# Optimization experiments

Hardware: AMD Instinct MI355X
Metric: run time of the kernel (lower is better)

## Reference

```python
import jax, jax.numpy as jnp
import numpy as np

D_IN, D, N_HEADS, K, VOCAB = 768, 512, 8, 6, 1000
HEAD_DIM = D // N_HEADS


def setup_inputs() -> dict:
    key = jax.random.key(0)
    ks = jax.random.split(key, 16)
    B, T, L = 32, 4096, 512
    s = 0.02
    return {
        "video_features": jax.random.normal(ks[0], (B, T, D_IN), jnp.float32),
        "input_ids": jax.random.randint(ks[1], (B, L), 0, VOCAB),
        "attention_mask": jnp.ones((B, L), jnp.float32),
        # video_encoder (Linear 768->512), stored [in, out]
        "W_enc": jax.random.normal(ks[2], (D_IN, D), jnp.float32) * s,
        "b_enc": jnp.zeros((D,), jnp.float32),
        # frame_selector (Linear 512->1)
        "W_sel": jax.random.normal(ks[3], (D, 1), jnp.float32) * s,
        "b_sel": jnp.zeros((1,), jnp.float32),
        # text_encoder embedding
        "emb": jax.random.normal(ks[4], (VOCAB, D), jnp.float32) * s,
        # MultiheadAttention in/out projections
        "W_q": jax.random.normal(ks[5], (D, D), jnp.float32) * s,
        "W_k": jax.random.normal(ks[6], (D, D), jnp.float32) * s,
        "W_v": jax.random.normal(ks[7], (D, D), jnp.float32) * s,
        "b_q": jnp.zeros((D,), jnp.float32),
        "b_k": jnp.zeros((D,), jnp.float32),
        "b_v": jnp.zeros((D,), jnp.float32),
        "W_o": jax.random.normal(ks[8], (D, D), jnp.float32) * s,
        "b_o": jnp.zeros((D,), jnp.float32),
        # classifier (Linear 512->1000)
        "W_cls": jax.random.normal(ks[9], (D, VOCAB), jnp.float32) * s,
        "b_cls": jnp.zeros((VOCAB,), jnp.float32),
    }


def reference(video_features, input_ids, attention_mask, W_enc, b_enc, W_sel,
              b_sel, emb, W_q, W_k, W_v, b_q, b_k, b_v, W_o, b_o, W_cls, b_cls):
    # encode frames: [B, T, 512]
    ve = jax.nn.relu(jnp.einsum('bti,io->bto', video_features, W_enc) + b_enc)
    # frame scores [B, T] -> top-6 gather
    scores = jnp.einsum('btd,do->bto', ve, W_sel)[..., 0] + b_sel[0]
    _, top_idx = jax.lax.top_k(scores, K)                      # [B, K]
    reps = jnp.take_along_axis(ve, top_idx[:, :, None], axis=1)  # [B, K, 512]
    # text embedding (query), reps as key/value
    txt = emb[input_ids]                                       # [B, L, 512]
    B, L, _ = txt.shape
    q = (txt @ W_q + b_q).reshape(B, L, N_HEADS, HEAD_DIM)
    k = (reps @ W_k + b_k).reshape(B, K, N_HEADS, HEAD_DIM)
    v = (reps @ W_v + b_v).reshape(B, K, N_HEADS, HEAD_DIM)
    scale = 1.0 / np.sqrt(HEAD_DIM).astype(np.float32)
    attn = jax.nn.softmax(jnp.einsum('blhd,bkhd->bhlk', q, k) * scale, axis=-1)
    ctx = jnp.einsum('bhlk,bkhd->blhd', attn, v).reshape(B, L, D)
    fused = ctx @ W_o + b_o
    logits = fused @ W_cls + b_cls                             # [B, L, 1000]
    return logits, reps
```

## Files before the change

### kernel.cpp

```cpp
#include <hip/hip_runtime.h>
#include <math.h>


#define DEV __device__ __forceinline__

typedef _Float16 half8 __attribute__((ext_vector_type(8)));
typedef float f32x4v __attribute__((ext_vector_type(4)));

DEV unsigned short f2h_bits(float f) {
  union { _Float16 h; unsigned short u; } cv;
  cv.h = (_Float16)f;
  return cv.u;
}

DEV void gload16(const void* g, void* lds) {
  auto* gp = reinterpret_cast<const __attribute__((address_space(1))) unsigned int*>(
      reinterpret_cast<unsigned long long>(g));
  auto* lp = reinterpret_cast<__attribute__((address_space(3))) unsigned int*>(
      reinterpret_cast<unsigned long long>(lds));
  __builtin_amdgcn_global_load_lds(gp, lp, 16, 0, 0);
}

__global__ __launch_bounds__(256) void wenct_k(const float* __restrict__ W_enc,
                                               unsigned short* __restrict__ WencT) {
  __shared__ unsigned short t[64][65];
  const int k0 = blockIdx.x * 64, n0 = blockIdx.y * 64, tid = threadIdx.x;
  for (int e = tid; e < 4096; e += 256) {
    int kk = e >> 6, nn = e & 63;
    t[kk][nn] = f2h_bits(W_enc[(size_t)(k0 + kk) * 512 + n0 + nn]);
  }
  __syncthreads();
  for (int e = tid; e < 4096; e += 256) {
    int nn = e >> 6, kk = e & 63;
    WencT[(size_t)(n0 + nn) * 768 + k0 + kk] = t[kk][nn];
  }
}

__global__ __launch_bounds__(512, 2) void score_gemm(
    const float* __restrict__ vf, const unsigned short* __restrict__ WencT,
    const float* __restrict__ b_enc, const float* __restrict__ W_sel,
    const float* __restrict__ b_sel, float* __restrict__ scores) {
  __shared__ unsigned short As[128 * 64];
  __shared__ unsigned short Bs[512 * 64];
  __shared__ float red[8 * 128];

  const int tid = threadIdx.x;
  const int w = tid >> 6, lane = tid & 63;
  const int quad = lane >> 4, l15 = lane & 15;
  const int rowBase = blockIdx.x * 128;
  const int swz = l15 & 7;
  char* const AsB = (char*)As;
  char* const BsB = (char*)Bs;

  f32x4v acc[8][4];
#pragma unroll
  for (int i = 0; i < 8; ++i)
#pragma unroll
    for (int j = 0; j < 4; ++j) acc[i][j] = (f32x4v){0.f, 0.f, 0.f, 0.f};

  const int ar0 = tid >> 3, as0 = tid & 7;

  for (int kk = 0; kk < 12; ++kk) {
    const int k0 = kk * 64;
    __syncthreads();
#pragma unroll
    for (int it = 0; it < 8; ++it) {
      int q = tid + it * 512;
      int n = q >> 3, seg = q & 7;
      gload16(WencT + (size_t)n * 768 + k0 + ((seg ^ (n & 7)) << 3),
              BsB + (it * 512 + w * 64) * 16);
    }
#pragma unroll
    for (int h = 0; h < 2; ++h) {
      int row = ar0 + h * 64;
      const float* src = vf + (size_t)(rowBase + row) * 768 + k0 + as0 * 8;
      float4 fa = *(const float4*)src;
      float4 fb = *(const float4*)(src + 4);
      uint4 pk;
      pk.x = f2h_bits(fa.x) | ((unsigned int)f2h_bits(fa.y) << 16);
      pk.y = f2h_bits(fa.z) | ((unsigned int)f2h_bits(fa.w) << 16);
      pk.z = f2h_bits(fb.x) | ((unsigned int)f2h_bits(fb.y) << 16);
      pk.w = f2h_bits(fb.z) | ((unsigned int)f2h_bits(fb.w) << 16);
      *(uint4*)(AsB + row * 128 + ((as0 ^ (row & 7)) << 4)) = pk;
    }
    __syncthreads();
#pragma unroll
    for (int c = 0; c < 2; ++c) {
      half8 af[8], bfr[4];
      const int so = (((c << 2) | quad) ^ swz) << 4;
#pragma unroll
      for (int i = 0; i < 8; ++i)
        af[i] = *(const half8*)(AsB + (16 * i + l15) * 128 + so);
#pragma unroll
      for (int j = 0; j < 4; ++j)
        bfr[j] = *(const half8*)(BsB + (w * 64 + 16 * j + l15) * 128 + so);
#pragma unroll
      for (int i = 0; i < 8; ++i)
#pragma unroll
        for (int j = 0; j < 4; ++j)
          acc[i][j] = __builtin_amdgcn_mfma_f32_16x16x32_f16(af[i], bfr[j], acc[i][j], 0, 0, 0);
    }
  }

  float be[4], wsv[4];
#pragma unroll
  for (int j = 0; j < 4; ++j) {
    int col = w * 64 + 16 * j + l15;
    be[j] = b_enc[col];
    wsv[j] = W_sel[col];
  }
  float part[32];
#pragma unroll
  for (int x = 0; x < 32; ++x) part[x] = 0.f;
#pragma unroll
  for (int i = 0; i < 8; ++i)
#pragma unroll
    for (int j = 0; j < 4; ++j)
#pragma unroll
      for (int r = 0; r < 4; ++r) {
        float v = acc[i][j][r] + be[j];
        v = fmaxf(v, 0.f);
        part[i * 4 + r] += v * wsv[j];
      }
#pragma unroll
  for (int m = 1; m < 16; m <<= 1)
#pragma unroll
    for (int x = 0; x < 32; ++x) part[x] += __shfl_xor(part[x], m);
  if (l15 == 0) {
#pragma unroll
    for (int i = 0; i < 8; ++i)
#pragma unroll
      for (int r = 0; r < 4; ++r)
        red[w * 128 + 16 * i + quad * 4 + r] = part[i * 4 + r];
  }
  __syncthreads();
  if (tid < 128) {
    float s = 0.f;
#pragma unroll
    for (int ww = 0; ww < 8; ++ww) s += red[ww * 128 + tid];
    scores[rowBase + tid] = s + b_sel[0];
  }
}

__global__ __launch_bounds__(256) void topk16(const float* __restrict__ scores,
                                              int* __restrict__ cand) {
  __shared__ float swv[4];
  __shared__ int swi[4];
  __shared__ int winner;
  const int b = blockIdx.x, tid = threadIdx.x;
  const int lane = tid & 63, w = tid >> 6;
  float v[16];
#pragma unroll
  for (int p = 0; p < 16; ++p) v[p] = scores[b * 4096 + p * 256 + tid];
  for (int r = 0; r < 16; ++r) {
    float bv = v[0];
    int bp = 0;
#pragma unroll
    for (int p = 1; p < 16; ++p)
      if (v[p] > bv) { bv = v[p]; bp = p; }
    int bi = bp * 256 + tid;
#pragma unroll
    for (int m = 1; m < 64; m <<= 1) {
      float ov = __shfl_xor(bv, m);
      int oi = __shfl_xor(bi, m);
      if (ov > bv || (ov == bv && oi < bi)) { bv = ov; bi = oi; }
    }
    if (lane == 0) { swv[w] = bv; swi[w] = bi; }
    __syncthreads();
    if (tid == 0) {
      float fv = swv[0];
      int fi = swi[0];
#pragma unroll
      for (int x = 1; x < 4; ++x)
        if (swv[x] > fv || (swv[x] == fv && swi[x] < fi)) { fv = swv[x]; fi = swi[x]; }
      cand[b * 16 + r] = fi;
      winner = fi;
    }
    __syncthreads();
    const int wi = winner;
    const int wp = wi >> 8, wt = wi & 255;
#pragma unroll
    for (int p = 0; p < 16; ++p)
      if (p == wp && tid == wt) v[p] = -3.0e38f;
    __syncthreads();
  }
}

__global__ __launch_bounds__(256) void rescore(
    const float* __restrict__ vf, const int* __restrict__ cand,
    const float* __restrict__ W_enc, const float* __restrict__ b_enc,
    const float* __restrict__ W_sel, const float* __restrict__ b_sel,
    float* __restrict__ veC, float* __restrict__ exsc) {
  __shared__ float vfs[4][768];
  __shared__ float redl[16];
  const int b = blockIdx.x, cb = blockIdx.y * 4, tid = threadIdx.x;
  for (int c = 0; c < 4; ++c) {
    int t = cand[b * 16 + cb + c];
    const float* src = vf + ((size_t)b * 4096 + t) * 768;
    for (int i = tid; i < 768; i += 256) vfs[c][i] = src[i];
  }
  __syncthreads();
  const int j0 = tid, j1 = tid + 256;
  float a0[4] = {0.f, 0.f, 0.f, 0.f}, a1[4] = {0.f, 0.f, 0.f, 0.f};
  for (int i = 0; i < 768; ++i) {
    float w0 = W_enc[(size_t)i * 512 + j0], w1 = W_enc[(size_t)i * 512 + j1];
#pragma unroll
    for (int c = 0; c < 4; ++c) {
      float x = vfs[c][i];
      a0[c] += x * w0;
      a1[c] += x * w1;
    }
  }
  float ws0 = W_sel[j0], ws1 = W_sel[j1];
  float be0 = b_enc[j0], be1 = b_enc[j1];
  float s[4];
#pragma unroll
  for (int c = 0; c < 4; ++c) {
    float v0 = fmaxf(a0[c] + be0, 0.f);
    float v1 = fmaxf(a1[c] + be1, 0.f);
    veC[((size_t)b * 16 + cb + c) * 512 + j0] = v0;
    veC[((size_t)b * 16 + cb + c) * 512 + j1] = v1;
    s[c] = v0 * ws0 + v1 * ws1;
  }
#pragma unroll
  for (int m = 1; m < 64; m <<= 1)
#pragma unroll
    for (int c = 0; c < 4; ++c) s[c] += __shfl_xor(s[c], m);
  int w = tid >> 6;
  if ((tid & 63) == 0) {
#pragma unroll
    for (int c = 0; c < 4; ++c) redl[c * 4 + w] = s[c];
  }
  __syncthreads();
  if (tid < 4)
    exsc[b * 16 + cb + tid] = redl[tid * 4 + 0] + redl[tid * 4 + 1] +
                              redl[tid * 4 + 2] + redl[tid * 4 + 3] + b_sel[0];
}

__global__ __launch_bounds__(256) void select6(
    const float* __restrict__ exsc, const int* __restrict__ cand,
    const float* __restrict__ veC, int* __restrict__ sel,
    float* __restrict__ repsOut) {
  __shared__ int selL[6];
  const int b = blockIdx.x, tid = threadIdx.x;
  if (tid == 0) {
    float v[16]; int idx[16]; bool used[16];
    for (int c = 0; c < 16; ++c) {
      v[c] = exsc[b * 16 + c];
      idx[c] = cand[b * 16 + c];
      used[c] = false;
    }
    for (int r = 0; r < 6; ++r) {
      int bi = -1;
      for (int c = 0; c < 16; ++c) {
        if (used[c]) continue;
        if (bi < 0 || v[c] > v[bi] || (v[c] == v[bi] && idx[c] < idx[bi])) bi = c;
      }
      used[bi] = true;
      selL[r] = bi;
      sel[b * 6 + r] = bi;
    }
  }
  __syncthreads();
  for (int r = 0; r < 6; ++r) {
    int c = selL[r];
    for (int i = tid; i < 512; i += 256)
      repsOut[((size_t)b * 6 + r) * 512 + i] = veC[((size_t)b * 16 + c) * 512 + i];
  }
}

__global__ __launch_bounds__(256) void kv_proj(
    const int* __restrict__ sel, const float* __restrict__ veC,
    const float* __restrict__ W_k, const float* __restrict__ W_v,
    const float* __restrict__ b_k, const float* __restrict__ b_v,
    float* __restrict__ Ks, float* __restrict__ Vs) {
  __shared__ float rep[512];
  const int br = blockIdx.x;
  const int b = br / 6;
  const int tid = threadIdx.x;
  const int c = sel[br];
  for (int i = tid; i < 512; i += 256) rep[i] = veC[((size_t)b * 16 + c) * 512 + i];
  __syncthreads();
  const int j0 = tid, j1 = tid + 256;
  float k0 = 0.f, k1 = 0.f, v0 = 0.f, v1 = 0.f;
  for (int m = 0; m < 512; ++m) {
    float x = rep[m];
    k0 += x * W_k[m * 512 + j0];
    k1 += x * W_k[m * 512 + j1];
    v0 += x * W_v[m * 512 + j0];
    v1 += x * W_v[m * 512 + j1];
  }
  Ks[(size_t)br * 512 + j0] = (k0 + b_k[j0]) * 0.125f;
  Ks[(size_t)br * 512 + j1] = (k1 + b_k[j1]) * 0.125f;
  Vs[(size_t)br * 512 + j0] = v0 + b_v[j0];
  Vs[(size_t)br * 512 + j1] = v1 + b_v[j1];
}

__global__ __launch_bounds__(256) void qemb_k(
    const float* __restrict__ emb, const float* __restrict__ W_q,
    const float* __restrict__ b_q, float* __restrict__ Qe) {
  __shared__ float er[4 * 512];
  const int r0 = blockIdx.x * 4, tid = threadIdx.x;
  for (int i = tid; i < 2048; i += 256) er[i] = emb[(size_t)r0 * 512 + i];
  __syncthreads();
  const int j0 = tid, j1 = tid + 256;
  float a0[4], a1[4];
#pragma unroll
  for (int r = 0; r < 4; ++r) { a0[r] = 0.f; a1[r] = 0.f; }
  for (int i = 0; i < 512; ++i) {
    float w0 = W_q[i * 512 + j0], w1 = W_q[i * 512 + j1];
#pragma unroll
    for (int r = 0; r < 4; ++r) {
      a0[r] += er[r * 512 + i] * w0;
      a1[r] += er[r * 512 + i] * w1;
    }
  }
  float bq0 = b_q[j0], bq1 = b_q[j1];
#pragma unroll
  for (int r = 0; r < 4; ++r) {
    Qe[(size_t)(r0 + r) * 512 + j0] = a0[r] + bq0;
    Qe[(size_t)(r0 + r) * 512 + j1] = a1[r] + bq1;
  }
}

__global__ __launch_bounds__(256) void woc_k(
    const float* __restrict__ W_o, const float* __restrict__ W_cls,
    unsigned short* __restrict__ WocT) {
  __shared__ float wr[4 * 512];
  const int i0 = blockIdx.x * 4, tid = threadIdx.x;
  for (int i = tid; i < 2048; i += 256) wr[i] = W_o[(size_t)i0 * 512 + i];
  __syncthreads();
  float a[4][4];
#pragma unroll
  for (int r = 0; r < 4; ++r)
#pragma unroll
    for (int c = 0; c < 4; ++c) a[r][c] = 0.f;
  for (int m = 0; m < 512; ++m) {
    float wc[4];
#pragma unroll
    for (int c = 0; c < 4; ++c) {
      int j = tid + c * 256;
      wc[c] = (j < 1000) ? W_cls[(size_t)m * 1000 + j] : 0.f;
    }
#pragma unroll
    for (int r = 0; r < 4; ++r) {
      float x = wr[r * 512 + m];
#pragma unroll
      for (int c = 0; c < 4; ++c) a[r][c] += x * wc[c];
    }
  }
#pragma unroll
  for (int r = 0; r < 4; ++r)
#pragma unroll
    for (int c = 0; c < 4; ++c) {
      int j = tid + c * 256;
      if (j < 1000) WocT[(size_t)j * 512 + i0 + r] = f2h_bits(a[r][c]);
    }
  if (blockIdx.x == 0) {
    for (int i = tid; i < 24 * 512; i += 256) WocT[512000 + i] = 0;
  }
}

__global__ void boc_k(const float* __restrict__ b_o, const float* __restrict__ W_cls,
                      const float* __restrict__ b_cls, float* __restrict__ boc) {
  int j = blockIdx.x * 256 + threadIdx.x;
  float s = 0.f;
  if (j < 1000) {
    for (int m = 0; m < 512; ++m) s += b_o[m] * W_cls[(size_t)m * 1000 + j];
    s += b_cls[j];
  }
  boc[j] = s;
}

__global__ __launch_bounds__(256) void ctx_kernel(
    const int* __restrict__ ids, const float* __restrict__ Qe,
    const float* __restrict__ Ks, const float* __restrict__ Vs,
    unsigned short* __restrict__ CTX) {
  const int token = blockIdx.x * 4 + (threadIdx.x >> 6);
  const int lane = threadIdx.x & 63;
  const int b = token >> 9;
  const int id = ids[token];
  float q[8];
#pragma unroll
  for (int h = 0; h < 8; ++h) q[h] = Qe[(size_t)id * 512 + h * 64 + lane];
  float s[8][6];
#pragma unroll
  for (int kk = 0; kk < 6; ++kk) {
    const float* kp = Ks + ((size_t)b * 6 + kk) * 512 + lane;
    float p[8];
#pragma unroll
    for (int h = 0; h < 8; ++h) p[h] = q[h] * kp[h * 64];
#pragma unroll
    for (int m = 1; m < 64; m <<= 1)
#pragma unroll
      for (int h = 0; h < 8; ++h) p[h] += __shfl_xor(p[h], m);
#pragma unroll
    for (int h = 0; h < 8; ++h) s[h][kk] = p[h];
  }
  const float* vbase = Vs + (size_t)b * 6 * 512 + lane;
#pragma unroll
  for (int h = 0; h < 8; ++h) {
    float mx = s[h][0];
#pragma unroll
    for (int kk = 1; kk < 6; ++kk) mx = fmaxf(mx, s[h][kk]);
    float e[6], sum = 0.f;
#pragma unroll
    for (int kk = 0; kk < 6; ++kk) { e[kk] = __expf(s[h][kk] - mx); sum += e[kk]; }
    float c = 0.f;
#pragma unroll
    for (int kk = 0; kk < 6; ++kk) c += e[kk] * vbase[(size_t)kk * 512 + h * 64];
    c *= (1.f / sum);
    CTX[(size_t)token * 512 + h * 64 + lane] = f2h_bits(c);
  }
}

__global__ __launch_bounds__(512, 2) void logits_gemm(
    const unsigned short* __restrict__ CTX, const unsigned short* __restrict__ WocT,
    const float* __restrict__ boc, float* __restrict__ out) {
  __shared__ unsigned short As[128 * 64];
  __shared__ unsigned short Bs[512 * 64];
  const int tid = threadIdx.x;
  const int w = tid >> 6, lane = tid & 63;
  const int quad = lane >> 4, l15 = lane & 15;
  const int rowBase = blockIdx.x * 128;
  const int n0 = blockIdx.y * 512;
  const int swz = l15 & 7;
  char* const AsB = (char*)As;
  char* const BsB = (char*)Bs;

  f32x4v acc[8][4];
#pragma unroll
  for (int i = 0; i < 8; ++i)
#pragma unroll
    for (int j = 0; j < 4; ++j) acc[i][j] = (f32x4v){0.f, 0.f, 0.f, 0.f};

  for (int kk = 0; kk < 8; ++kk) {
    const int k0 = kk * 64;
    __syncthreads();
#pragma unroll
    for (int h = 0; h < 2; ++h) {
      int u = tid + h * 512;
      int row = u >> 3, seg = u & 7;
      gload16(CTX + (size_t)(rowBase + row) * 512 + k0 + ((seg ^ (row & 7)) << 3),
              AsB + (h * 512 + w * 64) * 16);
    }
#pragma unroll
    for (int it = 0; it < 8; ++it) {
      int q = tid + it * 512;
      int n = q >> 3, seg = q & 7;
      gload16(WocT + (size_t)(n0 + n) * 512 + k0 + ((seg ^ (n & 7)) << 3),
              BsB + (it * 512 + w * 64) * 16);
    }
    __syncthreads();
#pragma unroll
    for (int c = 0; c < 2; ++c) {
      half8 af[8], bfr[4];
      const int so = (((c << 2) | quad) ^ swz) << 4;
#pragma unroll
      for (int i = 0; i < 8; ++i)
        af[i] = *(const half8*)(AsB + (16 * i + l15) * 128 + so);
#pragma unroll
      for (int j = 0; j < 4; ++j)
        bfr[j] = *(const half8*)(BsB + (w * 64 + 16 * j + l15) * 128 + so);
#pragma unroll
      for (int i = 0; i < 8; ++i)
#pragma unroll
        for (int j = 0; j < 4; ++j)
          acc[i][j] = __builtin_amdgcn_mfma_f32_16x16x32_f16(af[i], bfr[j], acc[i][j], 0, 0, 0);
    }
  }

  float bo[4];
#pragma unroll
  for (int j = 0; j < 4; ++j) bo[j] = boc[n0 + w * 64 + 16 * j + l15];
#pragma unroll
  for (int i = 0; i < 8; ++i)
#pragma unroll
    for (int j = 0; j < 4; ++j)
#pragma unroll
      for (int r = 0; r < 4; ++r) {
        int token = rowBase + 16 * i + quad * 4 + r;
        int col = n0 + w * 64 + 16 * j + l15;
        if (col < 1000) out[(size_t)token * 1000 + col] = acc[i][j][r] + bo[j];
      }
}

extern "C" void kernel_launch(void* const* d_in, const int* in_sizes, int n_in,
                              void* d_out, int out_size, void* d_ws, size_t ws_size,
                              hipStream_t stream) {
  (void)in_sizes; (void)n_in; (void)out_size; (void)ws_size;
  const float* vf    = (const float*)d_in[0];
  const int*   ids   = (const int*)d_in[1];
  const float* W_enc = (const float*)d_in[3];
  const float* b_enc = (const float*)d_in[4];
  const float* W_sel = (const float*)d_in[5];
  const float* b_sel = (const float*)d_in[6];
  const float* emb   = (const float*)d_in[7];
  const float* W_q   = (const float*)d_in[8];
  const float* W_k   = (const float*)d_in[9];
  const float* W_v   = (const float*)d_in[10];
  const float* b_q   = (const float*)d_in[11];
  const float* b_k   = (const float*)d_in[12];
  const float* b_v   = (const float*)d_in[13];
  const float* W_o   = (const float*)d_in[14];
  const float* b_o   = (const float*)d_in[15];
  const float* W_cls = (const float*)d_in[16];
  const float* b_cls = (const float*)d_in[17];

  float* out = (float*)d_out;
  float* reps_out = out + (size_t)16384000;

  char* p = (char*)d_ws;
  auto nxt = [&](size_t bytes) -> char* {
    char* q = p;
    p += (bytes + 255) & ~(size_t)255;
    return q;
  };
  unsigned short* WencT = (unsigned short*)nxt((size_t)512 * 768 * 2);
  unsigned short* WocT  = (unsigned short*)nxt((size_t)1024 * 512 * 2);
  unsigned short* CTX   = (unsigned short*)nxt((size_t)16384 * 512 * 2);
  float* scores = (float*)nxt((size_t)131072 * 4);
  int*   cand   = (int*)nxt((size_t)512 * 4);
  float* exsc   = (float*)nxt((size_t)512 * 4);
  float* veC    = (float*)nxt((size_t)32 * 16 * 512 * 4);
  int*   sel    = (int*)nxt((size_t)192 * 4);
  float* Ks     = (float*)nxt((size_t)98304 * 4);
  float* Vs     = (float*)nxt((size_t)98304 * 4);
  float* Qe     = (float*)nxt((size_t)512000 * 4);
  float* boc    = (float*)nxt((size_t)1024 * 4);

  hipLaunchKernelGGL(wenct_k,     dim3(12, 8),  dim3(256), 0, stream, W_enc, WencT);
  hipLaunchKernelGGL(score_gemm,  dim3(1024),   dim3(512), 0, stream, vf, WencT, b_enc, W_sel, b_sel, scores);
  hipLaunchKernelGGL(topk16,      dim3(32),     dim3(256), 0, stream, scores, cand);
  hipLaunchKernelGGL(rescore,     dim3(32, 4),  dim3(256), 0, stream, vf, cand, W_enc, b_enc, W_sel, b_sel, veC, exsc);
  hipLaunchKernelGGL(select6,     dim3(32),     dim3(256), 0, stream, exsc, cand, veC, sel, reps_out);
  hipLaunchKernelGGL(kv_proj,     dim3(192),    dim3(256), 0, stream, sel, veC, W_k, W_v, b_k, b_v, Ks, Vs);
  hipLaunchKernelGGL(qemb_k,      dim3(250),    dim3(256), 0, stream, emb, W_q, b_q, Qe);
  hipLaunchKernelGGL(woc_k,       dim3(128),    dim3(256), 0, stream, W_o, W_cls, WocT);
  hipLaunchKernelGGL(boc_k,       dim3(4),      dim3(256), 0, stream, b_o, W_cls, b_cls, boc);
  hipLaunchKernelGGL(ctx_kernel,  dim3(4096),   dim3(256), 0, stream, ids, Qe, Ks, Vs, CTX);
  hipLaunchKernelGGL(logits_gemm, dim3(128, 2), dim3(512), 0, stream, CTX, WocT, boc, out);
}
```

Before: 1.092 ms.

## Double-buffer GEMM K-loops and merge weight-prep kernels into one launch

Both MFMA GEMMs (score_gemm and logits_gemm) now use two LDS buffers with K-step 32 instead of a single buffer with K-step 64. The next tile is prefetched while the current one is consumed, with one barrier per step, so global loads overlap with compute. The four small weight-prep kernels (W_enc transpose, Q embedding projection, W_o·W_cls fusion, bias fold) are merged into a single launch dispatched by block index. This cuts launch overhead and lets these independent jobs run concurrently. In exchange there are twice as many loop iterations and barriers, and the swizzle pattern is narrower.

```diff
diff --git a/kernel.cpp b/kernel.cpp
--- a/kernel.cpp
+++ b/kernel.cpp
@@ -11,6 +11,15 @@
   union { _Float16 h; unsigned short u; } cv;
   cv.h = (_Float16)f;
   return cv.u;
+}
+
+DEV uint4 packf16x8(float4 fa, float4 fb) {
+  uint4 pk;
+  pk.x = (unsigned int)f2h_bits(fa.x) | ((unsigned int)f2h_bits(fa.y) << 16);
+  pk.y = (unsigned int)f2h_bits(fa.z) | ((unsigned int)f2h_bits(fa.w) << 16);
+  pk.z = (unsigned int)f2h_bits(fb.x) | ((unsigned int)f2h_bits(fb.y) << 16);
+  pk.w = (unsigned int)f2h_bits(fb.z) | ((unsigned int)f2h_bits(fb.w) << 16);
+  return pk;
 }
 
 DEV void gload16(const void* g, void* lds) {
@@ -21,18 +30,92 @@
   __builtin_amdgcn_global_load_lds(gp, lp, 16, 0, 0);
 }
 
-__global__ __launch_bounds__(256) void wenct_k(const float* __restrict__ W_enc,
-                                               unsigned short* __restrict__ WencT) {
-  __shared__ unsigned short t[64][65];
-  const int k0 = blockIdx.x * 64, n0 = blockIdx.y * 64, tid = threadIdx.x;
-  for (int e = tid; e < 4096; e += 256) {
-    int kk = e >> 6, nn = e & 63;
-    t[kk][nn] = f2h_bits(W_enc[(size_t)(k0 + kk) * 512 + n0 + nn]);
-  }
-  __syncthreads();
-  for (int e = tid; e < 4096; e += 256) {
-    int nn = e >> 6, kk = e & 63;
-    WencT[(size_t)(n0 + nn) * 768 + k0 + kk] = t[kk][nn];
+__global__ __launch_bounds__(256) void prep_k(
+    const float* __restrict__ W_enc, unsigned short* __restrict__ WencT,
+    const float* __restrict__ emb, const float* __restrict__ W_q,
+    const float* __restrict__ b_q, float* __restrict__ Qe,
+    const float* __restrict__ W_o, const float* __restrict__ W_cls,
+    unsigned short* __restrict__ WocT, const float* __restrict__ b_o,
+    const float* __restrict__ b_cls, float* __restrict__ boc) {
+  __shared__ float plds[2080];
+  const int blk = blockIdx.x, tid = threadIdx.x;
+  if (blk < 96) {
+    unsigned short* t = (unsigned short*)plds;
+    const int k0 = (blk % 12) * 64, n0 = (blk / 12) * 64;
+    for (int e = tid; e < 4096; e += 256) {
+      int kk = e >> 6, nn = e & 63;
+      t[kk * 65 + nn] = f2h_bits(W_enc[(size_t)(k0 + kk) * 512 + n0 + nn]);
+    }
+    __syncthreads();
+    for (int e = tid; e < 4096; e += 256) {
+      int nn = e >> 6, kk = e & 63;
+      WencT[(size_t)(n0 + nn) * 768 + k0 + kk] = t[kk * 65 + nn];
+    }
+  } else if (blk < 346) {
+    float* er = plds;
+    const int r0 = (blk - 96) * 4;
+    for (int i = tid; i < 2048; i += 256) er[i] = emb[(size_t)r0 * 512 + i];
+    __syncthreads();
+    const int j0 = tid, j1 = tid + 256;
+    float a0[4], a1[4];
+#pragma unroll
+    for (int r = 0; r < 4; ++r) { a0[r] = 0.f; a1[r] = 0.f; }
+    for (int i = 0; i < 512; ++i) {
+      float w0 = W_q[i * 512 + j0], w1 = W_q[i * 512 + j1];
+#pragma unroll
+      for (int r = 0; r < 4; ++r) {
+        a0[r] += er[r * 512 + i] * w0;
+        a1[r] += er[r * 512 + i] * w1;
+      }
+    }
+    float bq0 = b_q[j0], bq1 = b_q[j1];
+#pragma unroll
+    for (int r = 0; r < 4; ++r) {
+      Qe[(size_t)(r0 + r) * 512 + j0] = a0[r] + bq0;
+      Qe[(size_t)(r0 + r) * 512 + j1] = a1[r] + bq1;
+    }
+  } else if (blk < 474) {
+    float* wr = plds;
+    const int i0 = (blk - 346) * 4;
+    for (int i = tid; i < 2048; i += 256) wr[i] = W_o[(size_t)i0 * 512 + i];
+    __syncthreads();
+    float a[4][4];
+#pragma unroll
+    for (int r = 0; r < 4; ++r)
+#pragma unroll
+      for (int c = 0; c < 4; ++c) a[r][c] = 0.f;
+    for (int m = 0; m < 512; ++m) {
+      float wc[4];
+#pragma unroll
+      for (int c = 0; c < 4; ++c) {
+        int j = tid + c * 256;
+        wc[c] = (j < 1000) ? W_cls[(size_t)m * 1000 + j] : 0.f;
+      }
+#pragma unroll
+      for (int r = 0; r < 4; ++r) {
+        float x = wr[r * 512 + m];
+#pragma unroll
+        for (int c = 0; c < 4; ++c) a[r][c] += x * wc[c];
+      }
+    }
+#pragma unroll
+    for (int r = 0; r < 4; ++r)
+#pragma unroll
+      for (int c = 0; c < 4; ++c) {
+        int j = tid + c * 256;
+        if (j < 1000) WocT[(size_t)j * 512 + i0 + r] = f2h_bits(a[r][c]);
+      }
+    if (blk == 346) {
+      for (int i = tid; i < 24 * 512; i += 256) WocT[512000 + i] = 0;
+    }
+  } else {
+    int j = (blk - 474) * 256 + tid;
+    float s = 0.f;
+    if (j < 1000) {
+      for (int m = 0; m < 512; ++m) s += b_o[m] * W_cls[(size_t)m * 1000 + j];
+      s += b_cls[j];
+    }
+    boc[j] = s;
   }
 }
 
@@ -40,17 +123,19 @@
     const float* __restrict__ vf, const unsigned short* __restrict__ WencT,
     const float* __restrict__ b_enc, const float* __restrict__ W_sel,
     const float* __restrict__ b_sel, float* __restrict__ scores) {
-  __shared__ unsigned short As[128 * 64];
-  __shared__ unsigned short Bs[512 * 64];
+  __shared__ unsigned short As[2][128 * 32];
+  __shared__ unsigned short Bs[2][512 * 32];
   __shared__ float red[8 * 128];
 
   const int tid = threadIdx.x;
-  const int w = tid >> 6, lane = tid & 63;
+  const int wv = tid >> 6, lane = tid & 63;
   const int quad = lane >> 4, l15 = lane & 15;
   const int rowBase = blockIdx.x * 128;
-  const int swz = l15 & 7;
-  char* const AsB = (char*)As;
-  char* const BsB = (char*)Bs;
+  const int rso = ((quad ^ (l15 & 3)) << 4);
+  char* const AsB0 = (char*)As[0];
+  char* const AsB1 = (char*)As[1];
+  char* const BsB0 = (char*)Bs[0];
+  char* const BsB1 = (char*)Bs[1];
 
   f32x4v acc[8][4];
 #pragma unroll
@@ -58,54 +143,60 @@
 #pragma unroll
     for (int j = 0; j < 4; ++j) acc[i][j] = (f32x4v){0.f, 0.f, 0.f, 0.f};
 
-  const int ar0 = tid >> 3, as0 = tid & 7;
-
-  for (int kk = 0; kk < 12; ++kk) {
-    const int k0 = kk * 64;
-    __syncthreads();
-#pragma unroll
-    for (int it = 0; it < 8; ++it) {
+  const int arow = tid >> 2, aseg = tid & 3;
+  const float* aSrc = vf + (size_t)(rowBase + arow) * 768 + aseg * 8;
+  const int adst = arow * 64 + ((aseg ^ (arow & 3)) << 4);
+
+  auto stage_b = [&](int kk, char* dstB) {
+#pragma unroll
+    for (int it = 0; it < 4; ++it) {
       int q = tid + it * 512;
-      int n = q >> 3, seg = q & 7;
-      gload16(WencT + (size_t)n * 768 + k0 + ((seg ^ (n & 7)) << 3),
-              BsB + (it * 512 + w * 64) * 16);
-    }
-#pragma unroll
-    for (int h = 0; h < 2; ++h) {
-      int row = ar0 + h * 64;
-      const float* src = vf + (size_t)(rowBase + row) * 768 + k0 + as0 * 8;
-      float4 fa = *(const float4*)src;
-      float4 fb = *(const float4*)(src + 4);
-      uint4 pk;
-      pk.x = f2h_bits(fa.x) | ((unsigned int)f2h_bits(fa.y) << 16);
-      pk.y = f2h_bits(fa.z) | ((unsigned int)f2h_bits(fa.w) << 16);
-      pk.z = f2h_bits(fb.x) | ((unsigned int)f2h_bits(fb.y) << 16);
-      pk.w = f2h_bits(fb.z) | ((unsigned int)f2h_bits(fb.w) << 16);
-      *(uint4*)(AsB + row * 128 + ((as0 ^ (row & 7)) << 4)) = pk;
-    }
-    __syncthreads();
-#pragma unroll
-    for (int c = 0; c < 2; ++c) {
-      half8 af[8], bfr[4];
-      const int so = (((c << 2) | quad) ^ swz) << 4;
-#pragma unroll
-      for (int i = 0; i < 8; ++i)
-        af[i] = *(const half8*)(AsB + (16 * i + l15) * 128 + so);
+      int n = q >> 2, seg = q & 3;
+      gload16(WencT + (size_t)n * 768 + kk * 32 + ((seg ^ (n & 3)) << 3),
+              dstB + (it * 512 + wv * 64) * 16);
+    }
+  };
+  auto consume = [&](const char* A, const char* B) {
+    half8 af[8], bf[4];
+#pragma unroll
+    for (int i = 0; i < 8; ++i)
+      af[i] = *(const half8*)(A + (16 * i + l15) * 64 + rso);
+#pragma unroll
+    for (int j = 0; j < 4; ++j)
+      bf[j] = *(const half8*)(B + (wv * 64 + 16 * j + l15) * 64 + rso);
+#pragma unroll
+    for (int i = 0; i < 8; ++i)
 #pragma unroll
       for (int j = 0; j < 4; ++j)
-        bfr[j] = *(const half8*)(BsB + (w * 64 + 16 * j + l15) * 128 + so);
-#pragma unroll
-      for (int i = 0; i < 8; ++i)
-#pragma unroll
-        for (int j = 0; j < 4; ++j)
-          acc[i][j] = __builtin_amdgcn_mfma_f32_16x16x32_f16(af[i], bfr[j], acc[i][j], 0, 0, 0);
-    }
-  }
+        acc[i][j] = __builtin_amdgcn_mfma_f32_16x16x32_f16(af[i], bf[j], acc[i][j], 0, 0, 0);
+  };
+
+  stage_b(0, BsB0);
+  {
+    float4 fa = *(const float4*)(aSrc);
+    float4 fb = *(const float4*)(aSrc + 4);
+    *(uint4*)(AsB0 + adst) = packf16x8(fa, fb);
+  }
+  __syncthreads();
+  int cur = 0;
+  for (int kk = 0; kk < 23; ++kk) {
+    const float* s = aSrc + (kk + 1) * 32;
+    float4 fa = *(const float4*)(s);
+    float4 fb = *(const float4*)(s + 4);
+    char* An = cur ? AsB0 : AsB1;
+    char* Bn = cur ? BsB0 : BsB1;
+    stage_b(kk + 1, Bn);
+    consume(cur ? AsB1 : AsB0, cur ? BsB1 : BsB0);
+    *(uint4*)(An + adst) = packf16x8(fa, fb);
+    __syncthreads();
+    cur ^= 1;
+  }
+  consume(cur ? AsB1 : AsB0, cur ? BsB1 : BsB0);
 
   float be[4], wsv[4];
 #pragma unroll
   for (int j = 0; j < 4; ++j) {
-    int col = w * 64 + 16 * j + l15;
+    int col = wv * 64 + 16 * j + l15;
     be[j] = b_enc[col];
     wsv[j] = W_sel[col];
   }
@@ -131,7 +222,7 @@
     for (int i = 0; i < 8; ++i)
 #pragma unroll
       for (int r = 0; r < 4; ++r)
-        red[w * 128 + 16 * i + quad * 4 + r] = part[i * 4 + r];
+        red[wv * 128 + 16 * i + quad * 4 + r] = part[i * 4 + r];
   }
   __syncthreads();
   if (tid < 128) {
@@ -296,82 +387,6 @@
   Vs[(size_t)br * 512 + j1] = v1 + b_v[j1];
 }
 
-__global__ __launch_bounds__(256) void qemb_k(
-    const float* __restrict__ emb, const float* __restrict__ W_q,
-    const float* __restrict__ b_q, float* __restrict__ Qe) {
-  __shared__ float er[4 * 512];
-  const int r0 = blockIdx.x * 4, tid = threadIdx.x;
-  for (int i = tid; i < 2048; i += 256) er[i] = emb[(size_t)r0 * 512 + i];
-  __syncthreads();
-  const int j0 = tid, j1 = tid + 256;
-  float a0[4], a1[4];
-#pragma unroll
-  for (int r = 0; r < 4; ++r) { a0[r] = 0.f; a1[r] = 0.f; }
-  for (int i = 0; i < 512; ++i) {
-    float w0 = W_q[i * 512 + j0], w1 = W_q[i * 512 + j1];
-#pragma unroll
-    for (int r = 0; r < 4; ++r) {
-      a0[r] += er[r * 512 + i] * w0;
-      a1[r] += er[r * 512 + i] * w1;
-    }
-  }
-  float bq0 = b_q[j0], bq1 = b_q[j1];
-#pragma unroll
-  for (int r = 0; r < 4; ++r) {
-    Qe[(size_t)(r0 + r) * 512 + j0] = a0[r] + bq0;
-    Qe[(size_t)(r0 + r) * 512 + j1] = a1[r] + bq1;
-  }
-}
-
-__global__ __launch_bounds__(256) void woc_k(
-    const float* __restrict__ W_o, const float* __restrict__ W_cls,
-    unsigned short* __restrict__ WocT) {
-  __shared__ float wr[4 * 512];
-  const int i0 = blockIdx.x * 4, tid = threadIdx.x;
-  for (int i = tid; i < 2048; i += 256) wr[i] = W_o[(size_t)i0 * 512 + i];
-  __syncthreads();
-  float a[4][4];
-#pragma unroll
-  for (int r = 0; r < 4; ++r)
-#pragma unroll
-    for (int c = 0; c < 4; ++c) a[r][c] = 0.f;
-  for (int m = 0; m < 512; ++m) {
-    float wc[4];
-#pragma unroll
-    for (int c = 0; c < 4; ++c) {
-      int j = tid + c * 256;
-      wc[c] = (j < 1000) ? W_cls[(size_t)m * 1000 + j] : 0.f;
-    }
-#pragma unroll
-    for (int r = 0; r < 4; ++r) {
-      float x = wr[r * 512 + m];
-#pragma unroll
-      for (int c = 0; c < 4; ++c) a[r][c] += x * wc[c];
-    }
-  }
-#pragma unroll
-  for (int r = 0; r < 4; ++r)
-#pragma unroll
-    for (int c = 0; c < 4; ++c) {
-      int j = tid + c * 256;
-      if (j < 1000) WocT[(size_t)j * 512 + i0 + r] = f2h_bits(a[r][c]);
-    }
-  if (blockIdx.x == 0) {
-    for (int i = tid; i < 24 * 512; i += 256) WocT[512000 + i] = 0;
-  }
-}
-
-__global__ void boc_k(const float* __restrict__ b_o, const float* __restrict__ W_cls,
-                      const float* __restrict__ b_cls, float* __restrict__ boc) {
-  int j = blockIdx.x * 256 + threadIdx.x;
-  float s = 0.f;
-  if (j < 1000) {
-    for (int m = 0; m < 512; ++m) s += b_o[m] * W_cls[(size_t)m * 1000 + j];
-    s += b_cls[j];
-  }
-  boc[j] = s;
-}
-
 __global__ __launch_bounds__(256) void ctx_kernel(
     const int* __restrict__ ids, const float* __restrict__ Qe,
     const float* __restrict__ Ks, const float* __restrict__ Vs,
@@ -417,16 +432,18 @@
 __global__ __launch_bounds__(512, 2) void logits_gemm(
     const unsigned short* __restrict__ CTX, const unsigned short* __restrict__ WocT,
     const float* __restrict__ boc, float* __restrict__ out) {
-  __shared__ unsigned short As[128 * 64];
-  __shared__ unsigned short Bs[512 * 64];
+  __shared__ unsigned short As[2][128 * 32];
+  __shared__ unsigned short Bs[2][512 * 32];
   const int tid = threadIdx.x;
-  const int w = tid >> 6, lane = tid & 63;
+  const int wv = tid >> 6, lane = tid & 63;
   const int quad = lane >> 4, l15 = lane & 15;
   const int rowBase = blockIdx.x * 128;
   const int n0 = blockIdx.y * 512;
-  const int swz = l15 & 7;
-  char* const AsB = (char*)As;
-  char* const BsB = (char*)Bs;
+  const int rso = ((quad ^ (l15 & 3)) << 4);
+  char* const AsB0 = (char*)As[0];
+  char* const AsB1 = (char*)As[1];
+  char* const BsB0 = (char*)Bs[0];
+  char* const BsB1 = (char*)Bs[1];
 
   f32x4v acc[8][4];
 #pragma unroll
@@ -434,45 +451,49 @@
 #pragma unroll
     for (int j = 0; j < 4; ++j) acc[i][j] = (f32x4v){0.f, 0.f, 0.f, 0.f};
 
-  for (int kk = 0; kk < 8; ++kk) {
-    const int k0 = kk * 64;
-    __syncthreads();
-#pragma unroll
-    for (int h = 0; h < 2; ++h) {
-      int u = tid + h * 512;
-      int row = u >> 3, seg = u & 7;
-      gload16(CTX + (size_t)(rowBase + row) * 512 + k0 + ((seg ^ (row & 7)) << 3),
-              AsB + (h * 512 + w * 64) * 16);
-    }
-#pragma unroll
-    for (int it = 0; it < 8; ++it) {
+  const int arow = tid >> 2, aseg = tid & 3;
+
+  auto stage = [&](int kk, char* An, char* Bn) {
+    const int k0 = kk * 32;
+    gload16(CTX + (size_t)(rowBase + arow) * 512 + k0 + ((aseg ^ (arow & 3)) << 3),
+            An + (wv * 64) * 16);
+#pragma unroll
+    for (int it = 0; it < 4; ++it) {
       int q = tid + it * 512;
-      int n = q >> 3, seg = q & 7;
-      gload16(WocT + (size_t)(n0 + n) * 512 + k0 + ((seg ^ (n & 7)) << 3),
-              BsB + (it * 512 + w * 64) * 16);
-    }
-    __syncthreads();
-#pragma unroll
-    for (int c = 0; c < 2; ++c) {
-      half8 af[8], bfr[4];
-      const int so = (((c << 2) | quad) ^ swz) << 4;
-#pragma unroll
-      for (int i = 0; i < 8; ++i)
-        af[i] = *(const half8*)(AsB + (16 * i + l15) * 128 + so);
+      int n = q >> 2, seg = q & 3;
+      gload16(WocT + (size_t)(n0 + n) * 512 + k0 + ((seg ^ (n & 3)) << 3),
+              Bn + (it * 512 + wv * 64) * 16);
+    }
+  };
+  auto consume = [&](const char* A, const char* B) {
+    half8 af[8], bf[4];
+#pragma unroll
+    for (int i = 0; i < 8; ++i)
+      af[i] = *(const half8*)(A + (16 * i + l15) * 64 + rso);
+#pragma unroll
+    for (int j = 0; j < 4; ++j)
+      bf[j] = *(const half8*)(B + (wv * 64 + 16 * j + l15) * 64 + rso);
+#pragma unroll
+    for (int i = 0; i < 8; ++i)
 #pragma unroll
       for (int j = 0; j < 4; ++j)
-        bfr[j] = *(const half8*)(BsB + (w * 64 + 16 * j + l15) * 128 + so);
-#pragma unroll
-      for (int i = 0; i < 8; ++i)
-#pragma unroll
-        for (int j = 0; j < 4; ++j)
-          acc[i][j] = __builtin_amdgcn_mfma_f32_16x16x32_f16(af[i], bfr[j], acc[i][j], 0, 0, 0);
-    }
-  }
+        acc[i][j] = __builtin_amdgcn_mfma_f32_16x16x32_f16(af[i], bf[j], acc[i][j], 0, 0, 0);
+  };
+
+  stage(0, AsB0, BsB0);
+  __syncthreads();
+  int cur = 0;
+  for (int kk = 0; kk < 15; ++kk) {
+    stage(kk + 1, cur ? AsB0 : AsB1, cur ? BsB0 : BsB1);
+    consume(cur ? AsB1 : AsB0, cur ? BsB1 : BsB0);
+    __syncthreads();
+    cur ^= 1;
+  }
+  consume(cur ? AsB1 : AsB0, cur ? BsB1 : BsB0);
 
   float bo[4];
 #pragma unroll
-  for (int j = 0; j < 4; ++j) bo[j] = boc[n0 + w * 64 + 16 * j + l15];
+  for (int j = 0; j < 4; ++j) bo[j] = boc[n0 + wv * 64 + 16 * j + l15];
 #pragma unroll
   for (int i = 0; i < 8; ++i)
 #pragma unroll
@@ -480,7 +501,7 @@
 #pragma unroll
       for (int r = 0; r < 4; ++r) {
         int token = rowBase + 16 * i + quad * 4 + r;
-        int col = n0 + w * 64 + 16 * j + l15;
+        int col = n0 + wv * 64 + 16 * j + l15;
         if (col < 1000) out[(size_t)token * 1000 + col] = acc[i][j][r] + bo[j];
       }
 }
@@ -529,15 +550,15 @@
   float* Qe     = (float*)nxt((size_t)512000 * 4);
   float* boc    = (float*)nxt((size_t)1024 * 4);
 
-  hipLaunchKernelGGL(wenct_k,     dim3(12, 8),  dim3(256), 0, stream, W_enc, WencT);
-  hipLaunchKernelGGL(score_gemm,  dim3(1024),   dim3(512), 0, stream, vf, WencT, b_enc, W_sel, b_sel, scores);
+  hipLaunchKernelGGL(prep_k,      dim3(478),    dim3(256), 0, stream,
+                     W_enc, WencT, emb, W_q, b_q, Qe, W_o, W_cls, WocT, b_o, b_cls, boc);
+  hipLaunchKernelGGL(score_gemm,  dim3(1024),   dim3(512), 0, stream,
+                     vf, WencT, b_enc, W_sel, b_sel, scores);
   hipLaunchKernelGGL(topk16,      dim3(32),     dim3(256), 0, stream, scores, cand);
-  hipLaunchKernelGGL(rescore,     dim3(32, 4),  dim3(256), 0, stream, vf, cand, W_enc, b_enc, W_sel, b_sel, veC, exsc);
+  hipLaunchKernelGGL(rescore,     dim3(32, 4),  dim3(256), 0, stream,
+                     vf, cand, W_enc, b_enc, W_sel, b_sel, veC, exsc);
   hipLaunchKernelGGL(select6,     dim3(32),     dim3(256), 0, stream, exsc, cand, veC, sel, reps_out);
   hipLaunchKernelGGL(kv_proj,     dim3(192),    dim3(256), 0, stream, sel, veC, W_k, W_v, b_k, b_v, Ks, Vs);
-  hipLaunchKernelGGL(qemb_k,      dim3(250),    dim3(256), 0, stream, emb, W_q, b_q, Qe);
-  hipLaunchKernelGGL(woc_k,       dim3(128),    dim3(256), 0, stream, W_o, W_cls, WocT);
-  hipLaunchKernelGGL(boc_k,       dim3(4),      dim3(256), 0, stream, b_o, W_cls, b_cls, boc);
   hipLaunchKernelGGL(ctx_kernel,  dim3(4096),   dim3(256), 0, stream, ids, Qe, Ks, Vs, CTX);
   hipLaunchKernelGGL(logits_gemm, dim3(128, 2), dim3(512), 0, stream, CTX, WocT, boc, out);
 }
```

Result: faster. 979.5 us (-10.3%).
